# Kernel optimization log

Hardware: AMD Instinct MI355X
Metric: run time of the kernel (lower is better)

The kernel has to match this reference:

```python
import jax, jax.numpy as jnp
import numpy as np

B, C, N, K, OUT = 4, 192, 10000, 16, 384

def setup_inputs() -> dict:
    key = jax.random.key(0)
    k1, k2, k3, k4 = jax.random.split(key, 4)
    x = jax.random.normal(k1, (B, C, N, 1), dtype=jnp.float32)
    edge_index = jax.random.randint(k2, (2, B, N, K), 0, N, dtype=jnp.int32)
    # 1x1x1 Conv3d weight [OUT, 2C, 1, 1, 1] collapsed to [OUT, 2C]
    fan_in = 2 * C
    weight = jax.random.normal(k3, (OUT, 2 * C), dtype=jnp.float32) / np.sqrt(fan_in)
    bias = jax.random.normal(k4, (OUT,), dtype=jnp.float32) * 0.01
    return {"x": x, "edge_index": edge_index, "weight": weight, "bias": bias}


def _gather_neighbors(x3, idx):
    # x3: [B, C, N], idx: [B, N, K] -> [B, C, N, K]
    return jax.vmap(lambda xb, ib: xb[:, ib])(x3, idx)


def reference(x, edge_index, weight, bias):
    b, c, n, _ = x.shape
    x3 = x[..., 0]                                   # [B, C, N]
    x_i = _gather_neighbors(x3, edge_index[1])       # centers  [B, C, N, K]
    x_j = _gather_neighbors(x3, edge_index[0])       # neighbors [B, C, N, K]
    x_j_max = jnp.max(x_j - x_i, axis=-1)            # max-relative, [B, C, N]
    # torch.cat([x.unsqueeze(2), x_j.unsqueeze(2)], 2).reshape(b, 2c, n, 1)
    # interleaves channels as (x_c, xj_c) pairs
    feat = jnp.stack([x3, x_j_max], axis=2).reshape(b, 2 * c, n)  # [B, 2C, N]
    out = jnp.einsum('oc,bcn->bon', weight, feat) + bias[None, :, None]
    out = jax.nn.relu(out)
    # Conv3d path: output shape [B, OUT, N, 1, 1]
    return out[..., None, None]
```

## Files before the change

kernel.cpp:

```cpp
#include <hip/hip_runtime.h>


#define NB   4
#define NC   192
#define NN   10000
#define NK   16
#define NOUT 384
#define K2C  384

typedef short bf16x8 __attribute__((ext_vector_type(8)));
typedef float f32x4  __attribute__((ext_vector_type(4)));

__device__ inline unsigned short f2bf(float f) {
    unsigned int u = __builtin_bit_cast(unsigned int, f);
    u += ((u >> 16) & 1u) + 0x7FFFu;
    return (unsigned short)(u >> 16);
}
__device__ inline float bflo(unsigned int u) {
    return __builtin_bit_cast(float, u << 16);
}
__device__ inline float bfhi(unsigned int u) {
    return __builtin_bit_cast(float, u & 0xFFFF0000u);
}
__device__ inline unsigned long long uq(unsigned long long a) {
    unsigned int lo = __builtin_amdgcn_readfirstlane((unsigned int)a);
    unsigned int hi = __builtin_amdgcn_readfirstlane((unsigned int)(a >> 32));
    return ((unsigned long long)hi << 32) | lo;
}

__global__ __launch_bounds__(256) void k_prep(const float* __restrict__ x,
                                              unsigned short* __restrict__ xT,
                                              const float* __restrict__ w,
                                              unsigned short* __restrict__ wbf) {
    __shared__ unsigned short tile[NC * 65];
    int bid = blockIdx.x;
    if (bid >= 628) {
        int i = (bid - 628) * 256 + threadIdx.x;
        float4 v = ((const float4*)w)[i];
        uint2 o;
        o.x = (unsigned int)f2bf(v.x) | ((unsigned int)f2bf(v.y) << 16);
        o.y = (unsigned int)f2bf(v.z) | ((unsigned int)f2bf(v.w) << 16);
        ((uint2*)wbf)[i] = o;
        return;
    }
    int b  = bid & 3;
    int nb = (bid >> 2) * 64;
    int t  = threadIdx.x;
    const float* xb = x + (size_t)b * NC * NN;
    for (int i = 0; i < 48; ++i) {
        int idx = i * 256 + t;
        int c  = idx >> 6;
        int nl = idx & 63;
        int n  = nb + nl;
        float v = (n < NN) ? xb[(size_t)c * NN + n] : 0.f;
        tile[c * 65 + nl] = f2bf(v);
    }
    __syncthreads();
    unsigned short* xTb = xT + (size_t)b * NN * NC;
    for (int i = 0; i < 48; ++i) {
        int idx = i * 256 + t;
        int nl  = idx / NC;
        int c   = idx - nl * NC;
        int n   = nb + nl;
        if (n < NN) xTb[(size_t)n * NC + c] = tile[c * 65 + nl];
    }
}

__global__ __launch_bounds__(256, 2) void k_fused(const unsigned short* __restrict__ xT,
                                                  const int* __restrict__ eidx,
                                                  const unsigned short* __restrict__ wbf,
                                                  const float* __restrict__ bias,
                                                  float* __restrict__ out) {
    __shared__ unsigned short lds[64 * 48 * 8];
    int bid  = blockIdx.x;
    int b    = bid & 3;
    int nt   = bid >> 2;
    int tid  = threadIdx.x;
    int wv   = tid >> 6;
    int lane = tid & 63;
    int r    = lane & 15;
    int q    = lane >> 4;
    int le   = (lane < 48) ? lane : (lane - 48);

    const uint2* xr2 = (const uint2*)(xT + (size_t)b * NN * NC);
    const int* ep0 = eidx + (size_t)b * NN * NK;
    const int* ep1 = eidx + (size_t)NB * NN * NK + (size_t)b * NN * NK;
    int gnb = nt * 64 + wv * 16;

    for (int it = 0; it < 16; ++it) {
        int n = gnb + it;
        if (n >= NN) break;
        const int*  pj = (const int*) uq((unsigned long long)(ep0 + (size_t)n * NK));
        const int*  pi = (const int*) uq((unsigned long long)(ep1 + (size_t)n * NK));
        const uint2* rc = (const uint2*)uq((unsigned long long)(xr2 + (size_t)n * 48));
        uint2 cv = rc[le];
        float m0 = -INFINITY, m1 = -INFINITY, m2 = -INFINITY, m3 = -INFINITY;
#pragma unroll
        for (int h = 0; h < 2; ++h) {
            int js[8], is_[8];
#pragma unroll
            for (int k = 0; k < 8; ++k) {
                js[k]  = pj[h * 8 + k];
                is_[k] = pi[h * 8 + k];
            }
            uint2 jv[8], iv[8];
#pragma unroll
            for (int k = 0; k < 8; ++k) {
                jv[k] = xr2[(size_t)js[k]  * 48 + le];
                iv[k] = xr2[(size_t)is_[k] * 48 + le];
            }
#pragma unroll
            for (int k = 0; k < 8; ++k) {
                m0 = fmaxf(m0, bflo(jv[k].x) - bflo(iv[k].x));
                m1 = fmaxf(m1, bfhi(jv[k].x) - bfhi(iv[k].x));
                m2 = fmaxf(m2, bflo(jv[k].y) - bflo(iv[k].y));
                m3 = fmaxf(m3, bfhi(jv[k].y) - bfhi(iv[k].y));
            }
        }
        if (lane < 48) {
            unsigned int d0 = (cv.x & 0xFFFFu) | ((unsigned int)f2bf(m0) << 16);
            unsigned int d1 = (cv.x >> 16)     | ((unsigned int)f2bf(m1) << 16);
            unsigned int d2 = (cv.y & 0xFFFFu) | ((unsigned int)f2bf(m2) << 16);
            unsigned int d3 = (cv.y >> 16)     | ((unsigned int)f2bf(m3) << 16);
            unsigned int nw = (unsigned int)(wv * 16 + it);
            unsigned int s  = nw * 48u + ((unsigned int)le + 3u * nw) % 48u;
            uint4 o; o.x = d0; o.y = d1; o.z = d2; o.w = d3;
            ((uint4*)lds)[s] = o;
        }
    }

    __syncthreads();

    const unsigned short* aptr = wbf + (size_t)(wv * 96 + r) * K2C + q * 8;

    unsigned int nbase[4], u0[4];
#pragma unroll
    for (int ni = 0; ni < 4; ++ni) {
        unsigned int n = ni * 16 + r;
        nbase[ni] = n * 48u;
        u0[ni] = ((unsigned int)q + 3u * n) % 48u;
    }

    f32x4 acc[6][4];
#pragma unroll
    for (int mi = 0; mi < 6; ++mi)
#pragma unroll
        for (int ni = 0; ni < 4; ++ni)
            acc[mi][ni] = (f32x4){0.f, 0.f, 0.f, 0.f};

#pragma unroll 2
    for (int t = 0; t < 12; ++t) {
        bf16x8 a[6], bb[4];
#pragma unroll
        for (int mi = 0; mi < 6; ++mi)
            a[mi] = *(const bf16x8*)(aptr + (size_t)mi * 16 * K2C + t * 32);
#pragma unroll
        for (int ni = 0; ni < 4; ++ni) {
            unsigned int u = u0[ni] + 4u * t;
            if (u >= 48u) u -= 48u;
            bb[ni] = *(const bf16x8*)(lds + (size_t)(nbase[ni] + u) * 8);
        }
#pragma unroll
        for (int mi = 0; mi < 6; ++mi)
#pragma unroll
            for (int ni = 0; ni < 4; ++ni)
                acc[mi][ni] = __builtin_amdgcn_mfma_f32_16x16x32_bf16(a[mi], bb[ni], acc[mi][ni], 0, 0, 0);
    }

    float* ob = out + (size_t)b * NOUT * NN;
#pragma unroll
    for (int mi = 0; mi < 6; ++mi) {
        int obase = wv * 96 + mi * 16 + q * 4;
#pragma unroll
        for (int ni = 0; ni < 4; ++ni) {
            int n = nt * 64 + ni * 16 + r;
            if (n < NN) {
#pragma unroll
                for (int rr = 0; rr < 4; ++rr) {
                    int o = obase + rr;
                    float val = acc[mi][ni][rr] + bias[o];
                    ob[(size_t)o * NN + n] = fmaxf(val, 0.f);
                }
            }
        }
    }
}

extern "C" void kernel_launch(void* const* d_in, const int* in_sizes, int n_in,
                              void* d_out, int out_size, void* d_ws, size_t ws_size,
                              hipStream_t stream) {
    const float* x    = (const float*)d_in[0];
    const int*   eidx = (const int*)d_in[1];
    const float* w    = (const float*)d_in[2];
    const float* bias = (const float*)d_in[3];
    float* out = (float*)d_out;

    unsigned short* xT  = (unsigned short*)d_ws;
    unsigned short* wbf = xT + (size_t)NB * NN * NC;

    hipLaunchKernelGGL(k_prep,  dim3(628 + 144), dim3(256), 0, stream, x, xT, w, wbf);
    hipLaunchKernelGGL(k_fused, dim3(4 * 157),   dim3(256), 0, stream, xT, eidx, wbf, bias, out);
}
```

Baseline: 198.2 us.

## Preload edge indices per wave in vector regs and broadcast via readlane

Instead of scalar-loading 32 edge indices per node inside the gather loop, each wave loads all 16 nodes' indices up front into a vector register array (lanes 0-15 for neighbors, 16-31 for centers), then extracts them with readlane. All 32 row gathers for a node are issued together rather than in two dependent halves, and lanes 48-63 no longer duplicate loads. This removes serialized index-load latency from the gather loop, at the cost of 16 extra VGPRs per lane under a launch bound of 2 blocks.

```diff
diff --git a/kernel.cpp b/kernel.cpp
--- a/kernel.cpp
+++ b/kernel.cpp
@@ -21,11 +21,6 @@
 }
 __device__ inline float bfhi(unsigned int u) {
     return __builtin_bit_cast(float, u & 0xFFFF0000u);
-}
-__device__ inline unsigned long long uq(unsigned long long a) {
-    unsigned int lo = __builtin_amdgcn_readfirstlane((unsigned int)a);
-    unsigned int hi = __builtin_amdgcn_readfirstlane((unsigned int)(a >> 32));
-    return ((unsigned long long)hi << 32) | lo;
 }
 
 __global__ __launch_bounds__(256) void k_prep(const float* __restrict__ x,
@@ -80,52 +75,67 @@
     int lane = tid & 63;
     int r    = lane & 15;
     int q    = lane >> 4;
-    int le   = (lane < 48) ? lane : (lane - 48);
 
     const uint2* xr2 = (const uint2*)(xT + (size_t)b * NN * NC);
     const int* ep0 = eidx + (size_t)b * NN * NK;
     const int* ep1 = eidx + (size_t)NB * NN * NK + (size_t)b * NN * NK;
     int gnb = nt * 64 + wv * 16;
 
+    const int* epsel = (lane & 16) ? ep1 : ep0;
+    int kslot = lane & 15;
+    int vv[16];
+#pragma unroll
     for (int it = 0; it < 16; ++it) {
         int n = gnb + it;
-        if (n >= NN) break;
-        const int*  pj = (const int*) uq((unsigned long long)(ep0 + (size_t)n * NK));
-        const int*  pi = (const int*) uq((unsigned long long)(ep1 + (size_t)n * NK));
-        const uint2* rc = (const uint2*)uq((unsigned long long)(xr2 + (size_t)n * 48));
-        uint2 cv = rc[le];
-        float m0 = -INFINITY, m1 = -INFINITY, m2 = -INFINITY, m3 = -INFINITY;
-#pragma unroll
-        for (int h = 0; h < 2; ++h) {
-            int js[8], is_[8];
-#pragma unroll
-            for (int k = 0; k < 8; ++k) {
-                js[k]  = pj[h * 8 + k];
-                is_[k] = pi[h * 8 + k];
+        vv[it] = (lane < 32 && n < NN) ? epsel[(size_t)n * NK + kslot] : 0;
+    }
+
+#pragma unroll
+    for (int it = 0; it < 16; ++it) {
+        int n = gnb + it;
+        if (n < NN) {
+            int nl = wv * 16 + it;
+            if (lane < 48) {
+                uint2 cv = xr2[(size_t)n * 48 + lane];
+                uint2 ja[8], ia[8], jb[8], ib[8];
+#pragma unroll
+                for (int k = 0; k < 8; ++k) {
+                    int j = __builtin_amdgcn_readlane(vv[it], k);
+                    int i = __builtin_amdgcn_readlane(vv[it], 16 + k);
+                    ja[k] = xr2[(size_t)j * 48 + lane];
+                    ia[k] = xr2[(size_t)i * 48 + lane];
+                }
+#pragma unroll
+                for (int k = 0; k < 8; ++k) {
+                    int j = __builtin_amdgcn_readlane(vv[it], 8 + k);
+                    int i = __builtin_amdgcn_readlane(vv[it], 24 + k);
+                    jb[k] = xr2[(size_t)j * 48 + lane];
+                    ib[k] = xr2[(size_t)i * 48 + lane];
+                }
+                float m0 = -INFINITY, m1 = -INFINITY, m2 = -INFINITY, m3 = -INFINITY;
+#pragma unroll
+                for (int k = 0; k < 8; ++k) {
+                    m0 = fmaxf(m0, bflo(ja[k].x) - bflo(ia[k].x));
+                    m1 = fmaxf(m1, bfhi(ja[k].x) - bfhi(ia[k].x));
+                    m2 = fmaxf(m2, bflo(ja[k].y) - bflo(ia[k].y));
+                    m3 = fmaxf(m3, bfhi(ja[k].y) - bfhi(ia[k].y));
+                }
+#pragma unroll
+                for (int k = 0; k < 8; ++k) {
+                    m0 = fmaxf(m0, bflo(jb[k].x) - bflo(ib[k].x));
+                    m1 = fmaxf(m1, bfhi(jb[k].x) - bfhi(ib[k].x));
+                    m2 = fmaxf(m2, bflo(jb[k].y) - bflo(ib[k].y));
+                    m3 = fmaxf(m3, bfhi(jb[k].y) - bfhi(ib[k].y));
+                }
+                unsigned int d0 = (cv.x & 0xFFFFu) | ((unsigned int)f2bf(m0) << 16);
+                unsigned int d1 = (cv.x >> 16)     | ((unsigned int)f2bf(m1) << 16);
+                unsigned int d2 = (cv.y & 0xFFFFu) | ((unsigned int)f2bf(m2) << 16);
+                unsigned int d3 = (cv.y >> 16)     | ((unsigned int)f2bf(m3) << 16);
+                unsigned int nw = (unsigned int)nl;
+                unsigned int s  = nw * 48u + ((unsigned int)lane + 3u * nw) % 48u;
+                uint4 o; o.x = d0; o.y = d1; o.z = d2; o.w = d3;
+                ((uint4*)lds)[s] = o;
             }
-            uint2 jv[8], iv[8];
-#pragma unroll
-            for (int k = 0; k < 8; ++k) {
-                jv[k] = xr2[(size_t)js[k]  * 48 + le];
-                iv[k] = xr2[(size_t)is_[k] * 48 + le];
-            }
-#pragma unroll
-            for (int k = 0; k < 8; ++k) {
-                m0 = fmaxf(m0, bflo(jv[k].x) - bflo(iv[k].x));
-                m1 = fmaxf(m1, bfhi(jv[k].x) - bfhi(iv[k].x));
-                m2 = fmaxf(m2, bflo(jv[k].y) - bflo(iv[k].y));
-                m3 = fmaxf(m3, bfhi(jv[k].y) - bfhi(iv[k].y));
-            }
-        }
-        if (lane < 48) {
-            unsigned int d0 = (cv.x & 0xFFFFu) | ((unsigned int)f2bf(m0) << 16);
-            unsigned int d1 = (cv.x >> 16)     | ((unsigned int)f2bf(m1) << 16);
-            unsigned int d2 = (cv.y & 0xFFFFu) | ((unsigned int)f2bf(m2) << 16);
-            unsigned int d3 = (cv.y >> 16)     | ((unsigned int)f2bf(m3) << 16);
-            unsigned int nw = (unsigned int)(wv * 16 + it);
-            unsigned int s  = nw * 48u + ((unsigned int)le + 3u * nw) % 48u;
-            uint4 o; o.x = d0; o.y = d1; o.z = d2; o.w = d3;
-            ((uint4*)lds)[s] = o;
         }
     }
 
```

After: 195.5 us. Within noise of the previous version (-1.4%).
